# Performance work log

Hardware: AMD Instinct MI355X
Metric: run time of the kernel (lower is better)

Reference implementation:

```python
import jax, jax.numpy as jnp
import numpy as np
import math

N, KZ, IFZ, AHZ, AFZ = 20000, 16, 256, 8, 32
EPS = 1e-5


def layernorm(x, g, b):
    m = jnp.mean(x, axis=-1, keepdims=True)
    v = jnp.mean((x - m) ** 2, axis=-1, keepdims=True)
    return (x - m) * jax.lax.rsqrt(v + EPS) * g + b


def rotate_half(x):
    x1, x2 = jnp.split(x, 2, axis=-1)
    return jnp.concatenate([-x2, x1], axis=-1)


def setup_inputs() -> dict:
    key = jax.random.key(0)
    ks = jax.random.split(key, 16)
    s = 1.0 / math.sqrt(IFZ)
    hf = AHZ * AFZ
    return {
        "x_1": jax.random.normal(ks[0], (N, IFZ), jnp.float32),
        "x_2": jax.random.normal(ks[1], (N, KZ, IFZ), jnp.float32),
        "pos_emb": jax.random.normal(ks[2], (N, AFZ), jnp.float32),
        "edge_index": jax.random.randint(ks[3], (N, KZ), 0, N),
        "Wq": jax.random.normal(ks[4], (IFZ, hf), jnp.float32) * s,
        "Wk": jax.random.normal(ks[5], (IFZ, hf), jnp.float32) * s,
        "Wv": jax.random.normal(ks[6], (IFZ, hf), jnp.float32) * s,
        "Wb": jax.random.normal(ks[7], (IFZ, AHZ), jnp.float32) * s,
        "bln_g": jnp.ones((IFZ,), jnp.float32),
        "bln_b": jnp.zeros((IFZ,), jnp.float32),
        "Wg": jax.random.normal(ks[8], (IFZ, hf), jnp.float32) * s,
        "bg": jnp.zeros((hf,), jnp.float32),
        "Wback": jax.random.normal(ks[9], (hf, IFZ), jnp.float32) / math.sqrt(hf),
        "bback": jnp.zeros((IFZ,), jnp.float32),
        "ln1_g": jnp.ones((IFZ,), jnp.float32),
        "ln1_b": jnp.zeros((IFZ,), jnp.float32),
    }


def reference(x_1, x_2, pos_emb, edge_index, Wq, Wk, Wv, Wb, bln_g, bln_b,
              Wg, bg, Wback, bback, ln1_g, ln1_b):
    n = x_1.shape[0]
    y_1 = x_1[edge_index]                                  # [N,kz,ifz] irregular gather
    q = (x_1 @ Wq).reshape(n, AHZ, AFZ)                    # [N,h,f]
    k = (y_1 @ Wk).reshape(n, KZ, AHZ, AFZ)                # [N,kz,h,f]
    # RoPE: rotate q by each node's own angles, k by gathered neighbor angles
    cos_q = jnp.cos(pos_emb)[:, None, :]                   # [N,1,f]
    sin_q = jnp.sin(pos_emb)[:, None, :]
    q = q * cos_q + rotate_half(q) * sin_q
    pe_n = pos_emb[edge_index]                             # [N,kz,f]
    cos_k = jnp.cos(pe_n)[:, :, None, :]                   # [N,kz,1,f]
    sin_k = jnp.sin(pe_n)[:, :, None, :]
    k = k * cos_k + rotate_half(k) * sin_k
    v = (y_1 @ Wv).reshape(n, KZ, AHZ, AFZ)
    bias_2 = layernorm(x_2, bln_g, bln_b) @ Wb             # [N,kz,h]
    gate = jax.nn.sigmoid(x_1 @ Wg + bg).reshape(n, AHZ, AFZ)
    scores = jnp.einsum('nhf,nkhf->nkh', q, k) / math.sqrt(AFZ) + bias_2
    w = jax.nn.softmax(scores, axis=1)                     # over kz neighbors
    out = gate * jnp.einsum('nkh,nkhf->nhf', w, v)         # [N,h,f]
    out = out.reshape(n, AHZ * AFZ) @ Wback + bback + math.sqrt(2.0) * x_1
    return layernorm(out, ln1_g, ln1_b)
```

## Files before the change

### kernel.cpp

```cpp
#include <hip/hip_runtime.h>
#include <math.h>

#define IFZ 256
#define KZ  16
#define AHZ 8
#define AFZ 32
#define HF  256

typedef _Float16 half8 __attribute__((ext_vector_type(8)));
typedef _Float16 half4 __attribute__((ext_vector_type(4)));
typedef float    f32x4 __attribute__((ext_vector_type(4)));

__global__ void prep_all(const float* __restrict__ w0, const float* __restrict__ w1,
                         const float* __restrict__ w2, const float* __restrict__ w3,
                         const float* __restrict__ w4, _Float16* __restrict__ out,
                         const float* __restrict__ g, const float* __restrict__ b,
                         const float* __restrict__ Wb,
                         _Float16* __restrict__ c1T, float* __restrict__ c23)
{
    const int m = blockIdx.y;
    if (m < 5) {
        int k = blockIdx.x;
        int c = threadIdx.x;
        const float* w = (m == 0) ? w0 : (m == 1) ? w1 : (m == 2) ? w2 : (m == 3) ? w3 : w4;
        out[(size_t)m * 65536 + (size_t)c * 256 + k] = (_Float16)w[(size_t)k * 256 + c];
        return;
    }
    if (blockIdx.x != 0) return;

    __shared__ float red[4][16];
    const int f = threadIdx.x;
    const int w = f >> 6, l = f & 63;
    const float gv = g[f], bv = b[f];
    float ph2[8], ph3[8];
    #pragma unroll
    for (int h = 0; h < 8; ++h) {
        float wv = Wb[(size_t)f * 8 + h];
        c1T[h * 256 + f] = (_Float16)(gv * wv);
        ph2[h] = gv * wv;
        ph3[h] = bv * wv;
    }
    c1T[8 * 256 + f] = (_Float16)1.0f;
    #pragma unroll
    for (int cc = 9; cc < 16; ++cc) c1T[cc * 256 + f] = (_Float16)0.0f;

    #pragma unroll
    for (int h = 0; h < 8; ++h) {
        #pragma unroll
        for (int o = 32; o > 0; o >>= 1) {
            ph2[h] += __shfl_xor(ph2[h], o);
            ph3[h] += __shfl_xor(ph3[h], o);
        }
        if (l == h) { red[w][h] = ph2[h]; red[w][8 + h] = ph3[h]; }
    }
    __syncthreads();
    if (f < 16) c23[f] = red[0][f] + red[1][f] + red[2][f] + red[3][f];
}

__launch_bounds__(256)
__global__ void gemm_qkvg(const float* __restrict__ A, const _Float16* __restrict__ WT,
                          const float* __restrict__ pe, const float* __restrict__ bg,
                          _Float16* __restrict__ QH, _Float16* __restrict__ KH,
                          _Float16* __restrict__ VH, _Float16* __restrict__ GH, int N)
{
    __shared__ _Float16 as[64][40];
    __shared__ _Float16 bs[4][64][40];

    const int tid = threadIdx.x;
    const int l   = tid & 63;
    const int w   = tid >> 6;
    const int n0  = blockIdx.x * 64;
    const int c0  = blockIdx.y * 64;

    f32x4 acc[4][4];
    #pragma unroll
    for (int m = 0; m < 4; ++m)
        #pragma unroll
        for (int b = 0; b < 4; ++b)
            { acc[m][b][0]=0.f; acc[m][b][1]=0.f; acc[m][b][2]=0.f; acc[m][b][3]=0.f; }

    const int srow = tid >> 2;
    const int sch  = (tid & 3) * 8;
    const size_t aoff = (size_t)(n0 + srow) * IFZ + sch;
    const size_t boff = (size_t)(c0 + srow) * IFZ + sch;
    const bool arow_ok = (n0 + srow < N);

    half8 av{}, bv0, bv1, bv2, bv3;
    if (arow_ok) {
        f32x4 a0 = *reinterpret_cast<const f32x4*>(A + aoff);
        f32x4 a1 = *reinterpret_cast<const f32x4*>(A + aoff + 4);
        av[0]=(_Float16)a0[0]; av[1]=(_Float16)a0[1]; av[2]=(_Float16)a0[2]; av[3]=(_Float16)a0[3];
        av[4]=(_Float16)a1[0]; av[5]=(_Float16)a1[1]; av[6]=(_Float16)a1[2]; av[7]=(_Float16)a1[3];
    }
    bv0 = *reinterpret_cast<const half8*>(WT + 0 * 65536 + boff);
    bv1 = *reinterpret_cast<const half8*>(WT + 1 * 65536 + boff);
    bv2 = *reinterpret_cast<const half8*>(WT + 2 * 65536 + boff);
    bv3 = *reinterpret_cast<const half8*>(WT + 3 * 65536 + boff);

    for (int kt = 0; kt < 8; ++kt) {
        __syncthreads();
        *reinterpret_cast<half8*>(&as[srow][sch])    = av;
        *reinterpret_cast<half8*>(&bs[0][srow][sch]) = bv0;
        *reinterpret_cast<half8*>(&bs[1][srow][sch]) = bv1;
        *reinterpret_cast<half8*>(&bs[2][srow][sch]) = bv2;
        *reinterpret_cast<half8*>(&bs[3][srow][sch]) = bv3;
        __syncthreads();

        half8 nav{}, nbv0{}, nbv1{}, nbv2{}, nbv3{};
        if (kt < 7) {
            const int k0 = (kt + 1) * 32;
            if (arow_ok) {
                f32x4 a0 = *reinterpret_cast<const f32x4*>(A + aoff + k0);
                f32x4 a1 = *reinterpret_cast<const f32x4*>(A + aoff + k0 + 4);
                nav[0]=(_Float16)a0[0]; nav[1]=(_Float16)a0[1]; nav[2]=(_Float16)a0[2]; nav[3]=(_Float16)a0[3];
                nav[4]=(_Float16)a1[0]; nav[5]=(_Float16)a1[1]; nav[6]=(_Float16)a1[2]; nav[7]=(_Float16)a1[3];
            }
            nbv0 = *reinterpret_cast<const half8*>(WT + 0 * 65536 + boff + k0);
            nbv1 = *reinterpret_cast<const half8*>(WT + 1 * 65536 + boff + k0);
            nbv2 = *reinterpret_cast<const half8*>(WT + 2 * 65536 + boff + k0);
            nbv3 = *reinterpret_cast<const half8*>(WT + 3 * 65536 + boff + k0);
        }

        half8 af = *reinterpret_cast<const half8*>(&as[16 * w + (l & 15)][8 * (l >> 4)]);
        #pragma unroll
        for (int m = 0; m < 4; ++m) {
            #pragma unroll
            for (int b = 0; b < 4; ++b) {
                half8 bf = *reinterpret_cast<const half8*>(&bs[m][16 * b + (l & 15)][8 * (l >> 4)]);
                acc[m][b] = __builtin_amdgcn_mfma_f32_16x16x32_f16(af, bf, acc[m][b], 0, 0, 0);
            }
        }
        av = nav; bv0 = nbv0; bv1 = nbv1; bv2 = nbv2; bv3 = nbv3;
    }

    #pragma unroll
    for (int r = 0; r < 4; ++r) {
        const int grow = n0 + 16 * w + ((l >> 4) << 2) + r;
        if (grow >= N) continue;
        float a0 = pe[(size_t)grow * AFZ + (l & 15)];
        float a1 = pe[(size_t)grow * AFZ + 16 + (l & 15)];
        float s0, c0f, s1, c1f;
        __sincosf(a0, &s0, &c0f);
        __sincosf(a1, &s1, &c1f);
        #pragma unroll
        for (int m = 0; m < 2; ++m) {
            _Float16* o = m ? KH : QH;
            #pragma unroll
            for (int pb = 0; pb < 4; pb += 2) {
                float v0 = acc[m][pb][r], v1 = acc[m][pb + 1][r];
                o[(size_t)grow * HF + c0 + 16 * pb       + (l & 15)] = (_Float16)(v0 * c0f - v1 * s0);
                o[(size_t)grow * HF + c0 + 16 * (pb + 1) + (l & 15)] = (_Float16)(v1 * c1f + v0 * s1);
            }
        }
        #pragma unroll
        for (int b = 0; b < 4; ++b)
            VH[(size_t)grow * HF + c0 + 16 * b + (l & 15)] = (_Float16)acc[2][b][r];
        #pragma unroll
        for (int b = 0; b < 4; ++b) {
            const int c = c0 + 16 * b + (l & 15);
            float v = acc[3][b][r] + bg[c];
            GH[(size_t)grow * HF + c] = (_Float16)(1.f / (1.f + __expf(-v)));
        }
    }
}

__launch_bounds__(256)
__global__ void attn_fused(const _Float16* __restrict__ Qh, const _Float16* __restrict__ Kh,
                           const _Float16* __restrict__ Vh, const _Float16* __restrict__ Gh,
                           const int* __restrict__ eidx, const float* __restrict__ x2,
                           const _Float16* __restrict__ c1T, const float* __restrict__ c23,
                           _Float16* __restrict__ AOh, int N)
{
    const int tid = threadIdx.x;
    const int l   = tid & 63;
    const int w   = tid >> 6;
    const int n   = blockIdx.x * 4 + w;
    if (n >= N) return;
    const int h = l >> 3;
    const int c = l & 15;
    const int p = l >> 4;

    const int ei_reg = eidx[(size_t)n * KZ + c];

    const float* xr = x2 + ((size_t)n * KZ + c) * IFZ + p * 8;
    f32x4 xv[16];
    #pragma unroll
    for (int kt = 0; kt < 8; ++kt) {
        xv[2 * kt]     = __builtin_nontemporal_load(reinterpret_cast<const f32x4*>(xr + kt * 32));
        xv[2 * kt + 1] = __builtin_nontemporal_load(reinterpret_cast<const f32x4*>(xr + kt * 32 + 4));
    }
    half8 bf[8];
    #pragma unroll
    for (int kt = 0; kt < 8; ++kt)
        bf[kt] = *reinterpret_cast<const half8*>(c1T + (size_t)c * 256 + kt * 32 + p * 8);

    f32x4 acc1 = {0.f, 0.f, 0.f, 0.f};
    f32x4 acc2 = {0.f, 0.f, 0.f, 0.f};
    #pragma unroll
    for (int kt = 0; kt < 8; ++kt) {
        f32x4 xa = xv[2 * kt], xb = xv[2 * kt + 1];
        half8 ax, ax2;
        ax[0] = (_Float16)xa[0]; ax[1] = (_Float16)xa[1];
        ax[2] = (_Float16)xa[2]; ax[3] = (_Float16)xa[3];
        ax[4] = (_Float16)xb[0]; ax[5] = (_Float16)xb[1];
        ax[6] = (_Float16)xb[2]; ax[7] = (_Float16)xb[3];
        ax2[0] = (_Float16)(xa[0] * xa[0]); ax2[1] = (_Float16)(xa[1] * xa[1]);
        ax2[2] = (_Float16)(xa[2] * xa[2]); ax2[3] = (_Float16)(xa[3] * xa[3]);
        ax2[4] = (_Float16)(xb[0] * xb[0]); ax2[5] = (_Float16)(xb[1] * xb[1]);
        ax2[6] = (_Float16)(xb[2] * xb[2]); ax2[7] = (_Float16)(xb[3] * xb[3]);
        acc1 = __builtin_amdgcn_mfma_f32_16x16x32_f16(ax,  bf[kt], acc1, 0, 0, 0);
        acc2 = __builtin_amdgcn_mfma_f32_16x16x32_f16(ax2, bf[kt], acc2, 0, 0, 0);
    }

    const float c2v = (c < 8) ? c23[c]     : 0.f;
    const float c3v = (c < 8) ? c23[8 + c] : 0.f;
    const int srcl = (l & 48) | 8;
    float bval[4];
    #pragma unroll
    for (int j = 0; j < 4; ++j) {
        float s1 = __shfl(acc1[j], srcl);
        float s2 = __shfl(acc2[j], srcl);
        float m    = s1 * (1.f / 256.f);
        float var  = s2 * (1.f / 256.f) - m * m;
        float rstd = rsqrtf(var + 1e-5f);
        bval[j] = rstd * (acc1[j] - m * c2v) + c3v;
    }

    half4 qh4 = *reinterpret_cast<const half4*>(Qh + (size_t)n * HF + 4 * l);
    const float q0 = (float)qh4[0], q1 = (float)qh4[1],
                q2 = (float)qh4[2], q3 = (float)qh4[3];

    float sc[16];
    #pragma unroll
    for (int e = 0; e < 16; ++e) {
        const int row = __shfl(ei_reg, e);
        half4 kh4 = *reinterpret_cast<const half4*>(Kh + (size_t)row * HF + 4 * l);
        float s = q0 * (float)kh4[0] + q1 * (float)kh4[1]
                + q2 * (float)kh4[2] + q3 * (float)kh4[3];
        s += __shfl_xor(s, 1); s += __shfl_xor(s, 2); s += __shfl_xor(s, 4);
        sc[e] = s * 0.17677669529663687f
              + __shfl(bval[e & 3], ((e >> 2) << 4) | h);
    }

    float m = sc[0];
    #pragma unroll
    for (int e = 1; e < 16; ++e) m = fmaxf(m, sc[e]);
    float sum = 0.f;
    #pragma unroll
    for (int e = 0; e < 16; ++e) { sc[e] = __expf(sc[e] - m); sum += sc[e]; }
    const float inv = 1.f / sum;

    float o0 = 0.f, o1 = 0.f, o2 = 0.f, o3 = 0.f;
    #pragma unroll
    for (int e = 0; e < 16; ++e) {
        const int row = __shfl(ei_reg, e);
        half4 vh4 = *reinterpret_cast<const half4*>(Vh + (size_t)row * HF + 4 * l);
        const float we = sc[e] * inv;
        o0 = fmaf(we, (float)vh4[0], o0);
        o1 = fmaf(we, (float)vh4[1], o1);
        o2 = fmaf(we, (float)vh4[2], o2);
        o3 = fmaf(we, (float)vh4[3], o3);
    }

    half4 gh4 = *reinterpret_cast<const half4*>(Gh + (size_t)n * HF + 4 * l);
    half4 oh;
    oh[0] = (_Float16)(o0 * (float)gh4[0]);
    oh[1] = (_Float16)(o1 * (float)gh4[1]);
    oh[2] = (_Float16)(o2 * (float)gh4[2]);
    oh[3] = (_Float16)(o3 * (float)gh4[3]);
    *reinterpret_cast<half4*>(AOh + (size_t)n * HF + 4 * l) = oh;
}

__launch_bounds__(256)
__global__ void gemm_back_ln(const _Float16* __restrict__ A, const _Float16* __restrict__ BT,
                             const float* __restrict__ bbk, const float* __restrict__ x1,
                             const float* __restrict__ g1, const float* __restrict__ b1,
                             float* __restrict__ out, int N)
{
    __shared__ _Float16 as[64][40];
    __shared__ _Float16 bs[256][40];

    const int tid = threadIdx.x;
    const int l   = tid & 63;
    const int w   = tid >> 6;
    const int n0  = blockIdx.x * 64;

    f32x4 acc[16];
    #pragma unroll
    for (int bb = 0; bb < 16; ++bb)
        { acc[bb][0]=0.f; acc[bb][1]=0.f; acc[bb][2]=0.f; acc[bb][3]=0.f; }

    const int srowA = tid >> 2;
    const int schA  = (tid & 3) * 8;
    const size_t aoff = (size_t)(n0 + srowA) * IFZ + schA;
    const size_t boff = (size_t)tid * IFZ;
    const bool arow_ok = (n0 + srowA < N);

    half8 av{}, bv[4];
    if (arow_ok) av = *reinterpret_cast<const half8*>(A + aoff);
    #pragma unroll
    for (int i = 0; i < 4; ++i)
        bv[i] = *reinterpret_cast<const half8*>(BT + boff + i * 8);

    for (int kt = 0; kt < 8; ++kt) {
        __syncthreads();
        *reinterpret_cast<half8*>(&as[srowA][schA]) = av;
        #pragma unroll
        for (int i = 0; i < 4; ++i)
            *reinterpret_cast<half8*>(&bs[tid][i * 8]) = bv[i];
        __syncthreads();

        half8 nav{};
        half8 nbv[4] = {half8{}, half8{}, half8{}, half8{}};
        if (kt < 7) {
            const int k0 = (kt + 1) * 32;
            if (arow_ok) nav = *reinterpret_cast<const half8*>(A + aoff + k0);
            #pragma unroll
            for (int i = 0; i < 4; ++i)
                nbv[i] = *reinterpret_cast<const half8*>(BT + boff + k0 + i * 8);
        }

        half8 af = *reinterpret_cast<const half8*>(&as[16 * w + (l & 15)][8 * (l >> 4)]);
        #pragma unroll
        for (int bb = 0; bb < 16; ++bb) {
            half8 bf = *reinterpret_cast<const half8*>(&bs[16 * bb + (l & 15)][8 * (l >> 4)]);
            acc[bb] = __builtin_amdgcn_mfma_f32_16x16x32_f16(af, bf, acc[bb], 0, 0, 0);
        }
        av = nav;
        #pragma unroll
        for (int i = 0; i < 4; ++i) bv[i] = nbv[i];
    }

    const int c15 = l & 15;
    const int p   = l >> 4;
    float bias_r[16], g_r[16], b_r[16];
    #pragma unroll
    for (int bb = 0; bb < 16; ++bb) {
        const int cc = 16 * bb + c15;
        bias_r[bb] = bbk[cc]; g_r[bb] = g1[cc]; b_r[bb] = b1[cc];
    }

    #pragma unroll
    for (int j = 0; j < 4; ++j) {
        const int grow = n0 + 16 * w + 4 * p + j;
        const bool ok  = grow < N;
        float v[16];
        float s = 0.f, qq = 0.f;
        #pragma unroll
        for (int bb = 0; bb < 16; ++bb) {
            const int cc = 16 * bb + c15;
            float t = acc[bb][j] + bias_r[bb]
                    + 1.4142135623730951f * (ok ? x1[(size_t)grow * IFZ + cc] : 0.f);
            v[bb] = t; s += t; qq += t * t;
        }
        s  += __shfl_xor(s, 1);  s  += __shfl_xor(s, 2);
        s  += __shfl_xor(s, 4);  s  += __shfl_xor(s, 8);
        qq += __shfl_xor(qq, 1); qq += __shfl_xor(qq, 2);
        qq += __shfl_xor(qq, 4); qq += __shfl_xor(qq, 8);
        const float m    = s * (1.f / 256.f);
        const float var  = qq * (1.f / 256.f) - m * m;
        const float rstd = rsqrtf(var + 1e-5f);
        if (ok) {
            #pragma unroll
            for (int bb = 0; bb < 16; ++bb) {
                const int cc = 16 * bb + c15;
                out[(size_t)grow * IFZ + cc] = (v[bb] - m) * rstd * g_r[bb] + b_r[bb];
            }
        }
    }
}

extern "C" void kernel_launch(void* const* d_in, const int* in_sizes, int n_in,
                              void* d_out, int out_size, void* d_ws, size_t ws_size,
                              hipStream_t stream)
{
    const float* x1   = (const float*)d_in[0];
    const float* x2   = (const float*)d_in[1];
    const float* pe   = (const float*)d_in[2];
    const int*   ei   = (const int*)d_in[3];
    const float* wq   = (const float*)d_in[4];
    const float* wk   = (const float*)d_in[5];
    const float* wv   = (const float*)d_in[6];
    const float* wb   = (const float*)d_in[7];
    const float* blng = (const float*)d_in[8];
    const float* blnb = (const float*)d_in[9];
    const float* wg   = (const float*)d_in[10];
    const float* bg   = (const float*)d_in[11];
    const float* wbk  = (const float*)d_in[12];
    const float* bbk  = (const float*)d_in[13];
    const float* g1   = (const float*)d_in[14];
    const float* b1   = (const float*)d_in[15];

    const int N = in_sizes[0] / IFZ;

    const size_t S2 = (((size_t)N * HF * 2) + 4095) & ~(size_t)4095;
    char* base = (char*)d_ws;
    _Float16* QH  = (_Float16*)(base);
    _Float16* KH  = (_Float16*)(base + 1 * S2);
    _Float16* VH  = (_Float16*)(base + 2 * S2);
    _Float16* GH  = (_Float16*)(base + 3 * S2);
    _Float16* WT  = (_Float16*)(base + 4 * S2);
    _Float16* C1T = (_Float16*)(base + 4 * S2 + (1u << 20));
    float*    C23 = (float*)   (base + 4 * S2 + (1u << 20) + 8192);
    _Float16* AOH = QH;

    prep_all<<<dim3(256, 6), 256, 0, stream>>>(wq, wk, wv, wg, wbk, WT,
                                               blng, blnb, wb, C1T, C23);

    const int nt = (N + 63) / 64;
    gemm_qkvg<<<dim3(nt, 4), 256, 0, stream>>>(x1, WT, pe, bg, QH, KH, VH, GH, N);

    attn_fused<<<dim3((N + 3) / 4), 256, 0, stream>>>(QH, KH, VH, GH, ei, x2,
                                                      C1T, C23, AOH, N);

    gemm_back_ln<<<dim3(nt), 256, 0, stream>>>(AOH, WT + 4 * 65536, bbk, x1, g1, b1,
                                               (float*)d_out, N);
}
```

Baseline: 179.7 us.

## Split back-projection GEMM columns across waves with 16-row tiles and LDS LayerNorm reduction

The output GEMM+LayerNorm kernel now handles 16 rows per block instead of 64, and each wave computes 64 of the 256 output columns rather than a full 16-row strip. This gives four times as many blocks (about 1250) for better CU occupancy and fewer accumulator registers per thread. Row statistics are now combined across waves through a small shared-memory reduction. In exchange, every block reloads the full Wback matrix into LDS, so total B-operand traffic per row rises fourfold, and two extra barriers are added.

```diff
diff --git a/kernel.cpp b/kernel.cpp
--- a/kernel.cpp
+++ b/kernel.cpp
@@ -277,34 +277,36 @@
                              const float* __restrict__ g1, const float* __restrict__ b1,
                              float* __restrict__ out, int N)
 {
-    __shared__ _Float16 as[64][40];
+    __shared__ _Float16 as[16][40];
     __shared__ _Float16 bs[256][40];
+    __shared__ float red[4][16][2];
 
     const int tid = threadIdx.x;
     const int l   = tid & 63;
     const int w   = tid >> 6;
-    const int n0  = blockIdx.x * 64;
-
-    f32x4 acc[16];
-    #pragma unroll
-    for (int bb = 0; bb < 16; ++bb)
-        { acc[bb][0]=0.f; acc[bb][1]=0.f; acc[bb][2]=0.f; acc[bb][3]=0.f; }
-
-    const int srowA = tid >> 2;
-    const int schA  = (tid & 3) * 8;
-    const size_t aoff = (size_t)(n0 + srowA) * IFZ + schA;
+    const int n0  = blockIdx.x * 16;
+    const int c15 = l & 15;
+    const int p   = l >> 4;
+
+    f32x4 acc[4];
+    #pragma unroll
+    for (int b = 0; b < 4; ++b) { acc[b][0]=0.f; acc[b][1]=0.f; acc[b][2]=0.f; acc[b][3]=0.f; }
+
+    const int arow = tid >> 2;
+    const int ach  = (tid & 3) * 8;
+    const size_t aoff = (size_t)(n0 + arow) * IFZ + ach;
     const size_t boff = (size_t)tid * IFZ;
-    const bool arow_ok = (n0 + srowA < N);
+    const bool astage = (tid < 64) && (n0 + arow < N);
 
     half8 av{}, bv[4];
-    if (arow_ok) av = *reinterpret_cast<const half8*>(A + aoff);
+    if (astage) av = *reinterpret_cast<const half8*>(A + aoff);
     #pragma unroll
     for (int i = 0; i < 4; ++i)
         bv[i] = *reinterpret_cast<const half8*>(BT + boff + i * 8);
 
     for (int kt = 0; kt < 8; ++kt) {
         __syncthreads();
-        *reinterpret_cast<half8*>(&as[srowA][schA]) = av;
+        if (tid < 64) *reinterpret_cast<half8*>(&as[arow & 15][ach]) = av;
         #pragma unroll
         for (int i = 0; i < 4; ++i)
             *reinterpret_cast<half8*>(&bs[tid][i * 8]) = bv[i];
@@ -314,58 +316,70 @@
         half8 nbv[4] = {half8{}, half8{}, half8{}, half8{}};
         if (kt < 7) {
             const int k0 = (kt + 1) * 32;
-            if (arow_ok) nav = *reinterpret_cast<const half8*>(A + aoff + k0);
+            if (astage) nav = *reinterpret_cast<const half8*>(A + aoff + k0);
             #pragma unroll
             for (int i = 0; i < 4; ++i)
                 nbv[i] = *reinterpret_cast<const half8*>(BT + boff + k0 + i * 8);
         }
 
-        half8 af = *reinterpret_cast<const half8*>(&as[16 * w + (l & 15)][8 * (l >> 4)]);
-        #pragma unroll
-        for (int bb = 0; bb < 16; ++bb) {
-            half8 bf = *reinterpret_cast<const half8*>(&bs[16 * bb + (l & 15)][8 * (l >> 4)]);
-            acc[bb] = __builtin_amdgcn_mfma_f32_16x16x32_f16(af, bf, acc[bb], 0, 0, 0);
+        half8 af = *reinterpret_cast<const half8*>(&as[c15][8 * p]);
+        #pragma unroll
+        for (int b = 0; b < 4; ++b) {
+            half8 bf = *reinterpret_cast<const half8*>(&bs[64 * w + 16 * b + c15][8 * p]);
+            acc[b] = __builtin_amdgcn_mfma_f32_16x16x32_f16(af, bf, acc[b], 0, 0, 0);
         }
         av = nav;
         #pragma unroll
         for (int i = 0; i < 4; ++i) bv[i] = nbv[i];
     }
 
-    const int c15 = l & 15;
-    const int p   = l >> 4;
-    float bias_r[16], g_r[16], b_r[16];
-    #pragma unroll
-    for (int bb = 0; bb < 16; ++bb) {
-        const int cc = 16 * bb + c15;
-        bias_r[bb] = bbk[cc]; g_r[bb] = g1[cc]; b_r[bb] = b1[cc];
-    }
-
+    float v[4][4];
+    float sj[4], qj[4];
+    #pragma unroll
+    for (int j = 0; j < 4; ++j) { sj[j] = 0.f; qj[j] = 0.f; }
     #pragma unroll
     for (int j = 0; j < 4; ++j) {
-        const int grow = n0 + 16 * w + 4 * p + j;
+        const int grow = n0 + 4 * p + j;
         const bool ok  = grow < N;
-        float v[16];
-        float s = 0.f, qq = 0.f;
-        #pragma unroll
-        for (int bb = 0; bb < 16; ++bb) {
-            const int cc = 16 * bb + c15;
-            float t = acc[bb][j] + bias_r[bb]
+        #pragma unroll
+        for (int b = 0; b < 4; ++b) {
+            const int cc = 64 * w + 16 * b + c15;
+            float t = acc[b][j] + bbk[cc]
                     + 1.4142135623730951f * (ok ? x1[(size_t)grow * IFZ + cc] : 0.f);
-            v[bb] = t; s += t; qq += t * t;
-        }
-        s  += __shfl_xor(s, 1);  s  += __shfl_xor(s, 2);
-        s  += __shfl_xor(s, 4);  s  += __shfl_xor(s, 8);
-        qq += __shfl_xor(qq, 1); qq += __shfl_xor(qq, 2);
-        qq += __shfl_xor(qq, 4); qq += __shfl_xor(qq, 8);
+            v[b][j] = t; sj[j] += t; qj[j] += t * t;
+        }
+    }
+    #pragma unroll
+    for (int j = 0; j < 4; ++j) {
+        sj[j] += __shfl_xor(sj[j], 1); sj[j] += __shfl_xor(sj[j], 2);
+        sj[j] += __shfl_xor(sj[j], 4); sj[j] += __shfl_xor(sj[j], 8);
+        qj[j] += __shfl_xor(qj[j], 1); qj[j] += __shfl_xor(qj[j], 2);
+        qj[j] += __shfl_xor(qj[j], 4); qj[j] += __shfl_xor(qj[j], 8);
+    }
+    __syncthreads();
+    if (c15 == 0) {
+        #pragma unroll
+        for (int j = 0; j < 4; ++j) {
+            red[w][4 * p + j][0] = sj[j];
+            red[w][4 * p + j][1] = qj[j];
+        }
+    }
+    __syncthreads();
+
+    #pragma unroll
+    for (int j = 0; j < 4; ++j) {
+        const int row16 = 4 * p + j;
+        const int grow  = n0 + row16;
+        if (grow >= N) continue;
+        float s  = red[0][row16][0] + red[1][row16][0] + red[2][row16][0] + red[3][row16][0];
+        float qq = red[0][row16][1] + red[1][row16][1] + red[2][row16][1] + red[3][row16][1];
         const float m    = s * (1.f / 256.f);
         const float var  = qq * (1.f / 256.f) - m * m;
         const float rstd = rsqrtf(var + 1e-5f);
-        if (ok) {
-            #pragma unroll
-            for (int bb = 0; bb < 16; ++bb) {
-                const int cc = 16 * bb + c15;
-                out[(size_t)grow * IFZ + cc] = (v[bb] - m) * rstd * g_r[bb] + b_r[bb];
-            }
+        #pragma unroll
+        for (int b = 0; b < 4; ++b) {
+            const int cc = 64 * w + 16 * b + c15;
+            out[(size_t)grow * IFZ + cc] = (v[b][j] - m) * rstd * g1[cc] + b1[cc];
         }
     }
 }
@@ -413,6 +427,6 @@
     attn_fused<<<dim3((N + 3) / 4), 256, 0, stream>>>(QH, KH, VH, GH, ei, x2,
                                                       C1T, C23, AOH, N);
 
-    gemm_back_ln<<<dim3(nt), 256, 0, stream>>>(AOH, WT + 4 * 65536, bbk, x1, g1, b1,
-                                               (float*)d_out, N);
+    gemm_back_ln<<<dim3((N + 15) / 16), 256, 0, stream>>>(AOH, WT + 4 * 65536, bbk,
+                                                          x1, g1, b1, (float*)d_out, N);
 }
```

Measured after the change: 180.9 us. No clear change (+0.7%).
